# Performance work log

Hardware: AMD Instinct MI355X
Metric: run time of the kernel (lower is better)

Reference implementation:

```python
import jax, jax.numpy as jnp
import numpy as np

N_HEADS = 16
NEG_BIAS = -1e9


def setup_inputs() -> dict:
    key = jax.random.key(0)
    kq, kk, kv = jax.random.split(key, 3)
    B, S, D = 2, 2048, 1024
    queries = jax.random.normal(kq, (B, S, D), dtype=jnp.float32)
    keys = jax.random.normal(kk, (B, S, D), dtype=jnp.float32)
    values = jax.random.normal(kv, (B, S, D), dtype=jnp.float32)
    # causal mask [B, S, S]: True = attend allowed
    mask = jnp.broadcast_to(jnp.tril(jnp.ones((S, S), dtype=bool)), (B, S, S))
    return {"queries": queries, "keys": keys, "values": values, "mask": mask}


def reference(queries, keys, values, mask):
    B, S, D = queries.shape
    H = N_HEADS
    dh = D // H

    def split_heads(t):  # [B,S,D] -> [B,H,S,dh]
        return t.reshape(B, -1, H, dh).transpose(0, 2, 1, 3)

    q = split_heads(queries)
    k = split_heads(keys)
    v = split_heads(values)

    # scaled dot-product similarity: [B,H,Sq,Sk]
    sim = jnp.einsum('bhqd,bhkd->bhqk', q, k) / jnp.sqrt(jnp.asarray(dh, q.dtype))

    # additive mask bias (mask rank 3 -> broadcast over heads)
    bias = NEG_BIAS * (~mask).astype(sim.dtype)  # [B,Sq,Sk]
    masked = sim + bias[:, None, :, :]

    # stable softmax (original subtracts row max then softmaxes)
    weights = jax.nn.softmax(masked, axis=-1)

    # dropout is identity at inference (rate=None -> 0)
    out = jnp.einsum('bhqk,bhkd->bhqd', weights, v)

    # combine heads: [B,H,S,dh] -> [B,S,D]
    out = out.transpose(0, 2, 1, 3).reshape(B, S, D)
    return out
```

## Files before the change

kernel.cpp:

```cpp
#include <hip/hip_runtime.h>

#define B_ 2
#define S_ 2048
#define D_ 1024
#define H_ 16
#define DH 64
#define KB 64
#define SCALE 0.125f

typedef _Float16 f16x8 __attribute__((ext_vector_type(8)));
typedef _Float16 f16x4 __attribute__((ext_vector_type(4)));
typedef float f32x4 __attribute__((ext_vector_type(4)));


__global__ __launch_bounds__(256, 2) void mha_fwd(
    const float* __restrict__ qg, const float* __restrict__ kg,
    const float* __restrict__ vg, float* __restrict__ out)
{
  __shared__ __align__(16) _Float16 lds_k[KB * DH];
  __shared__ __align__(16) _Float16 lds_v[DH * KB];

  int bx = blockIdx.x;
  int L  = (bx & 7) * 64 + (bx >> 3);
  int bh  = L >> 4;
  int qbp = L & 15;
  int h = bh & 15;
  int b = bh >> 4;

  int tid  = threadIdx.x;
  int wid  = tid >> 6;
  int lane = tid & 63;
  int n    = lane & 15;
  int g    = lane >> 4;

  const float* qbase = qg + (size_t)b * S_ * D_ + h * DH;
  const float* kbase = kg + (size_t)b * S_ * D_ + h * DH;
  const float* vbase = vg + (size_t)b * S_ * D_ + h * DH;

  const int skey  = tid >> 2;
  const int spart = tid & 3;
  const int vdh   = tid & 63;
  const int vkq   = tid >> 6;

  float4 kf[4];
  float  vf[16];

  for (int ph = 0; ph < 2; ++ph) {
    const int qb   = ph ? (31 - qbp) : qbp;
    const int nkt  = qb + 1;
    const int qrow = qb * 64 + wid * 16;

    f16x8 bq[2];
    {
      const float* qp = qbase + (size_t)(qrow + n) * D_ + g * 8;
#pragma unroll
      for (int c = 0; c < 2; ++c) {
        float4 x0 = *(const float4*)(qp + c * 32);
        float4 x1 = *(const float4*)(qp + c * 32 + 4);
        f16x8 a;
        a[0]=(_Float16)(x0.x*SCALE); a[1]=(_Float16)(x0.y*SCALE);
        a[2]=(_Float16)(x0.z*SCALE); a[3]=(_Float16)(x0.w*SCALE);
        a[4]=(_Float16)(x1.x*SCALE); a[5]=(_Float16)(x1.y*SCALE);
        a[6]=(_Float16)(x1.z*SCALE); a[7]=(_Float16)(x1.w*SCALE);
        bq[c] = a;
      }
    }

    f32x4 o_acc[4] = {};
    float m_run = -1e30f, l_run = 0.f;

    {
      const float* kp = kbase + (size_t)skey * D_ + spart * 16;
#pragma unroll
      for (int i = 0; i < 4; ++i) kf[i] = ((const float4*)kp)[i];
      const float* vp = vbase + (size_t)(vkq * 16) * D_ + vdh;
#pragma unroll
      for (int j = 0; j < 16; ++j) vf[j] = vp[(size_t)j * D_];
    }

    for (int kt = 0; kt < nkt; ++kt) {
      __syncthreads();
      {
        const float* kfl = (const float*)kf;
        f16x8 h0, h1;
#pragma unroll
        for (int j = 0; j < 8; ++j) { h0[j] = (_Float16)kfl[j]; h1[j] = (_Float16)kfl[8+j]; }
        int c0 = spart * 2;
        *(f16x8*)((char*)lds_k + skey*128 + (((c0  ) ^ (skey&7))<<4)) = h0;
        *(f16x8*)((char*)lds_k + skey*128 + (((c0+1) ^ (skey&7))<<4)) = h1;
      }
      {
        f16x8 h0, h1;
#pragma unroll
        for (int j = 0; j < 8; ++j) { h0[j] = (_Float16)vf[j]; h1[j] = (_Float16)vf[8+j]; }
        int kb8 = vkq * 2;
        _Float16* vt = lds_v + vdh * 64;
        *(f16x8*)(vt + (((kb8  ) ^ (vdh&7)) << 3)) = h0;
        *(f16x8*)(vt + (((kb8+1) ^ (vdh&7)) << 3)) = h1;
      }
      __syncthreads();
      if (kt + 1 < nkt) {
        const float* kp = kbase + (size_t)((kt+1)*KB + skey) * D_ + spart * 16;
#pragma unroll
        for (int i = 0; i < 4; ++i) kf[i] = ((const float4*)kp)[i];
        const float* vp = vbase + (size_t)((kt+1)*KB + vkq*16) * D_ + vdh;
#pragma unroll
        for (int j = 0; j < 16; ++j) vf[j] = vp[(size_t)j * D_];
      }

      f32x4 sc[4] = {};
#pragma unroll
      for (int t = 0; t < 4; ++t) {
        int keyl = t * 16 + n;
#pragma unroll
        for (int c = 0; c < 2; ++c) {
          int off = keyl * 128 + (((c*4+g) ^ (keyl&7)) << 4);
          f16x8 ak = *(f16x8*)((char*)lds_k + off);
          sc[t] = __builtin_amdgcn_mfma_f32_16x16x32_f16(ak, bq[c], sc[t], 0, 0, 0);
        }
      }

      if (kt == nkt - 1) {
        int q = qrow + n;
#pragma unroll
        for (int t = 0; t < 4; ++t)
#pragma unroll
          for (int r = 0; r < 4; ++r) {
            int key = kt*KB + t*16 + 4*g + r;
            if (key > q) sc[t][r] = -1e30f;
          }
      }

      float mx = sc[0][0];
#pragma unroll
      for (int t = 0; t < 4; ++t)
#pragma unroll
        for (int r = 0; r < 4; ++r) mx = fmaxf(mx, sc[t][r]);
      mx = fmaxf(mx, __shfl_xor(mx, 16, 64));
      mx = fmaxf(mx, __shfl_xor(mx, 32, 64));
      float mnew  = fmaxf(m_run, mx);
      float alpha = __expf(m_run - mnew);
      m_run = mnew;
      float s = 0.f;
#pragma unroll
      for (int t = 0; t < 4; ++t)
#pragma unroll
        for (int r = 0; r < 4; ++r) {
          float p = __expf(sc[t][r] - mnew);
          sc[t][r] = p; s += p;
        }
      l_run = l_run * alpha + s;

      float ar[4];
#pragma unroll
      for (int r = 0; r < 4; ++r) ar[r] = __shfl(alpha, 4*g + r, 64);
#pragma unroll
      for (int nt = 0; nt < 4; ++nt) {
        f32x4 oa = o_acc[nt];
#pragma unroll
        for (int r = 0; r < 4; ++r) oa[r] *= ar[r];
        o_acc[nt] = oa;
      }

      f16x4 pa[4];
#pragma unroll
      for (int u = 0; u < 4; ++u) {
        f16x4 p4;
#pragma unroll
        for (int r = 0; r < 4; ++r) p4[r] = (_Float16)sc[u][r];
        pa[u] = p4;
      }

#pragma unroll
      for (int u = 0; u < 4; ++u) {
#pragma unroll
        for (int nt = 0; nt < 4; ++nt) {
          int dh  = nt*16 + n;
          int off = dh*64 + (((2*u + (g>>1)) ^ (n & 7)) << 3) + ((g & 1) << 2);
          f16x4 bv = *(f16x4*)(lds_v + off);
          o_acc[nt] = __builtin_amdgcn_mfma_f32_16x16x16f16(pa[u], bv, o_acc[nt], 0, 0, 0);
        }
      }
    }

    float lsum = l_run;
    lsum += __shfl_xor(lsum, 16, 64);
    lsum += __shfl_xor(lsum, 32, 64);
    float linv[4];
#pragma unroll
    for (int r = 0; r < 4; ++r) linv[r] = 1.0f / __shfl(lsum, 4*g + r, 64);

    float* ob = out + ((size_t)b * S_ + qrow) * D_ + h * DH;
#pragma unroll
    for (int r = 0; r < 4; ++r) {
      float* op = ob + (size_t)(4*g + r) * D_ + n;
#pragma unroll
      for (int nt = 0; nt < 4; ++nt)
        op[nt*16] = o_acc[nt][r] * linv[r];
    }
  }
}

extern "C" void kernel_launch(void* const* d_in, const int* in_sizes, int n_in,
                              void* d_out, int out_size, void* d_ws, size_t ws_size,
                              hipStream_t stream) {
  const float* q = (const float*)d_in[0];
  const float* k = (const float*)d_in[1];
  const float* v = (const float*)d_in[2];
  float* out = (float*)d_out;
  dim3 grid(512);
  mha_fwd<<<grid, 256, 0, stream>>>(q, k, v, out);
}
```

Before: 150.6 us.

## Double-buffer K/V tiles in LDS and add lazy softmax rescaling with exp2

K/V tiles now go into two LDS buffers. The next tile is loaded from global before compute and written to the other buffer afterward, which cuts the loop from two barriers to one. Softmax now uses exp2 with log2e folded into the Q scale. The running max is updated only when some lane's tile max exceeds it by more than a threshold, which skips most rescales of the output accumulator. s_setprio raises wave priority around the MFMA section; the trade-off is doubled LDS use and possible fp16 overflow risk bounded by the threshold.

```diff
diff --git a/kernel.cpp b/kernel.cpp
--- a/kernel.cpp
+++ b/kernel.cpp
@@ -6,7 +6,8 @@
 #define H_ 16
 #define DH 64
 #define KB 64
-#define SCALE 0.125f
+#define SCALE_LOG2 0.18033688011112042f
+#define THR 11.0f
 
 typedef _Float16 f16x8 __attribute__((ext_vector_type(8)));
 typedef _Float16 f16x4 __attribute__((ext_vector_type(4)));
@@ -17,8 +18,8 @@
     const float* __restrict__ qg, const float* __restrict__ kg,
     const float* __restrict__ vg, float* __restrict__ out)
 {
-  __shared__ __align__(16) _Float16 lds_k[KB * DH];
-  __shared__ __align__(16) _Float16 lds_v[DH * KB];
+  __shared__ __align__(16) _Float16 lds_k[2][KB * DH];
+  __shared__ __align__(16) _Float16 lds_v[2][DH * KB];
 
   int bx = blockIdx.x;
   int L  = (bx & 7) * 64 + (bx >> 3);
@@ -45,6 +46,33 @@
   float4 kf[4];
   float  vf[16];
 
+  auto load_tile = [&](int kt) {
+    const float* kp = kbase + (size_t)(kt * KB + skey) * D_ + spart * 16;
+#pragma unroll
+    for (int i = 0; i < 4; ++i) kf[i] = ((const float4*)kp)[i];
+    const float* vp = vbase + (size_t)(kt * KB + vkq * 16) * D_ + vdh;
+#pragma unroll
+    for (int j = 0; j < 16; ++j) vf[j] = vp[(size_t)j * D_];
+  };
+
+  auto store_tile = [&](int buf) {
+    const float* kfl = (const float*)kf;
+    f16x8 h0, h1;
+#pragma unroll
+    for (int j = 0; j < 8; ++j) { h0[j] = (_Float16)kfl[j]; h1[j] = (_Float16)kfl[8 + j]; }
+    int c0 = spart * 2;
+    char* kb_ = (char*)&lds_k[buf][0];
+    *(f16x8*)(kb_ + skey * 128 + (((c0    ) ^ (skey & 7)) << 4)) = h0;
+    *(f16x8*)(kb_ + skey * 128 + (((c0 + 1) ^ (skey & 7)) << 4)) = h1;
+    f16x8 v0, v1;
+#pragma unroll
+    for (int j = 0; j < 8; ++j) { v0[j] = (_Float16)vf[j]; v1[j] = (_Float16)vf[8 + j]; }
+    int kb8 = vkq * 2;
+    _Float16* vt = &lds_v[buf][0] + vdh * 64;
+    *(f16x8*)(vt + (((kb8    ) ^ (vdh & 7)) << 3)) = v0;
+    *(f16x8*)(vt + (((kb8 + 1) ^ (vdh & 7)) << 3)) = v1;
+  };
+
   for (int ph = 0; ph < 2; ++ph) {
     const int qb   = ph ? (31 - qbp) : qbp;
     const int nkt  = qb + 1;
@@ -58,64 +86,35 @@
         float4 x0 = *(const float4*)(qp + c * 32);
         float4 x1 = *(const float4*)(qp + c * 32 + 4);
         f16x8 a;
-        a[0]=(_Float16)(x0.x*SCALE); a[1]=(_Float16)(x0.y*SCALE);
-        a[2]=(_Float16)(x0.z*SCALE); a[3]=(_Float16)(x0.w*SCALE);
-        a[4]=(_Float16)(x1.x*SCALE); a[5]=(_Float16)(x1.y*SCALE);
-        a[6]=(_Float16)(x1.z*SCALE); a[7]=(_Float16)(x1.w*SCALE);
+        a[0]=(_Float16)(x0.x*SCALE_LOG2); a[1]=(_Float16)(x0.y*SCALE_LOG2);
+        a[2]=(_Float16)(x0.z*SCALE_LOG2); a[3]=(_Float16)(x0.w*SCALE_LOG2);
+        a[4]=(_Float16)(x1.x*SCALE_LOG2); a[5]=(_Float16)(x1.y*SCALE_LOG2);
+        a[6]=(_Float16)(x1.z*SCALE_LOG2); a[7]=(_Float16)(x1.w*SCALE_LOG2);
         bq[c] = a;
       }
     }
 
     f32x4 o_acc[4] = {};
-    float m_run = -1e30f, l_run = 0.f;
-
-    {
-      const float* kp = kbase + (size_t)skey * D_ + spart * 16;
-#pragma unroll
-      for (int i = 0; i < 4; ++i) kf[i] = ((const float4*)kp)[i];
-      const float* vp = vbase + (size_t)(vkq * 16) * D_ + vdh;
-#pragma unroll
-      for (int j = 0; j < 16; ++j) vf[j] = vp[(size_t)j * D_];
-    }
+    float m_run = 0.f, l_run = 0.f;
+
+    load_tile(0);
+    store_tile(0);
+    __syncthreads();
+    int cur = 0;
 
     for (int kt = 0; kt < nkt; ++kt) {
-      __syncthreads();
-      {
-        const float* kfl = (const float*)kf;
-        f16x8 h0, h1;
-#pragma unroll
-        for (int j = 0; j < 8; ++j) { h0[j] = (_Float16)kfl[j]; h1[j] = (_Float16)kfl[8+j]; }
-        int c0 = spart * 2;
-        *(f16x8*)((char*)lds_k + skey*128 + (((c0  ) ^ (skey&7))<<4)) = h0;
-        *(f16x8*)((char*)lds_k + skey*128 + (((c0+1) ^ (skey&7))<<4)) = h1;
-      }
-      {
-        f16x8 h0, h1;
-#pragma unroll
-        for (int j = 0; j < 8; ++j) { h0[j] = (_Float16)vf[j]; h1[j] = (_Float16)vf[8+j]; }
-        int kb8 = vkq * 2;
-        _Float16* vt = lds_v + vdh * 64;
-        *(f16x8*)(vt + (((kb8  ) ^ (vdh&7)) << 3)) = h0;
-        *(f16x8*)(vt + (((kb8+1) ^ (vdh&7)) << 3)) = h1;
-      }
-      __syncthreads();
-      if (kt + 1 < nkt) {
-        const float* kp = kbase + (size_t)((kt+1)*KB + skey) * D_ + spart * 16;
-#pragma unroll
-        for (int i = 0; i < 4; ++i) kf[i] = ((const float4*)kp)[i];
-        const float* vp = vbase + (size_t)((kt+1)*KB + vkq*16) * D_ + vdh;
-#pragma unroll
-        for (int j = 0; j < 16; ++j) vf[j] = vp[(size_t)j * D_];
-      }
-
+      if (kt + 1 < nkt) load_tile(kt + 1);
+
+      __builtin_amdgcn_s_setprio(1);
+      const char* kb_ = (const char*)&lds_k[cur][0];
       f32x4 sc[4] = {};
 #pragma unroll
       for (int t = 0; t < 4; ++t) {
         int keyl = t * 16 + n;
 #pragma unroll
         for (int c = 0; c < 2; ++c) {
-          int off = keyl * 128 + (((c*4+g) ^ (keyl&7)) << 4);
-          f16x8 ak = *(f16x8*)((char*)lds_k + off);
+          int off = keyl * 128 + (((c * 4 + g) ^ (keyl & 7)) << 4);
+          f16x8 ak = *(f16x8*)(kb_ + off);
           sc[t] = __builtin_amdgcn_mfma_f32_16x16x32_f16(ak, bq[c], sc[t], 0, 0, 0);
         }
       }
@@ -126,41 +125,48 @@
         for (int t = 0; t < 4; ++t)
 #pragma unroll
           for (int r = 0; r < 4; ++r) {
-            int key = kt*KB + t*16 + 4*g + r;
+            int key = kt * KB + t * 16 + 4 * g + r;
             if (key > q) sc[t][r] = -1e30f;
           }
       }
 
-      float mx = sc[0][0];
+      float mxt[4];
 #pragma unroll
       for (int t = 0; t < 4; ++t)
-#pragma unroll
-        for (int r = 0; r < 4; ++r) mx = fmaxf(mx, sc[t][r]);
+        mxt[t] = fmaxf(fmaxf(sc[t][0], sc[t][1]), fmaxf(sc[t][2], sc[t][3]));
+      float mx = fmaxf(fmaxf(mxt[0], mxt[1]), fmaxf(mxt[2], mxt[3]));
       mx = fmaxf(mx, __shfl_xor(mx, 16, 64));
       mx = fmaxf(mx, __shfl_xor(mx, 32, 64));
-      float mnew  = fmaxf(m_run, mx);
-      float alpha = __expf(m_run - mnew);
-      m_run = mnew;
+
       float s = 0.f;
 #pragma unroll
-      for (int t = 0; t < 4; ++t)
-#pragma unroll
-        for (int r = 0; r < 4; ++r) {
-          float p = __expf(sc[t][r] - mnew);
-          sc[t][r] = p; s += p;
-        }
-      l_run = l_run * alpha + s;
-
-      float ar[4];
-#pragma unroll
-      for (int r = 0; r < 4; ++r) ar[r] = __shfl(alpha, 4*g + r, 64);
-#pragma unroll
-      for (int nt = 0; nt < 4; ++nt) {
-        f32x4 oa = o_acc[nt];
-#pragma unroll
-        for (int r = 0; r < 4; ++r) oa[r] *= ar[r];
-        o_acc[nt] = oa;
-      }
+      for (int t = 0; t < 4; ++t) {
+        f32x4 p = sc[t];
+#pragma unroll
+        for (int r = 0; r < 4; ++r) p[r] = exp2f(p[r] - m_run);
+        sc[t] = p;
+        s += (p[0] + p[1]) + (p[2] + p[3]);
+      }
+
+      if (!__all(mx <= m_run + THR)) {
+        float mnew  = fmaxf(m_run, mx);
+        float alpha = exp2f(m_run - mnew);
+#pragma unroll
+        for (int t = 0; t < 4; ++t)
+#pragma unroll
+          for (int r = 0; r < 4; ++r) sc[t][r] *= alpha;
+        s *= alpha;
+        l_run *= alpha;
+        m_run = mnew;
+        float ar[4];
+#pragma unroll
+        for (int r = 0; r < 4; ++r) ar[r] = __shfl(alpha, 4 * g + r, 64);
+#pragma unroll
+        for (int nt = 0; nt < 4; ++nt)
+#pragma unroll
+          for (int r = 0; r < 4; ++r) o_acc[nt][r] *= ar[r];
+      }
+      l_run += s;
 
       f16x4 pa[4];
 #pragma unroll
@@ -171,16 +177,22 @@
         pa[u] = p4;
       }
 
+      const _Float16* vb_ = &lds_v[cur][0];
 #pragma unroll
       for (int u = 0; u < 4; ++u) {
 #pragma unroll
         for (int nt = 0; nt < 4; ++nt) {
-          int dh  = nt*16 + n;
-          int off = dh*64 + (((2*u + (g>>1)) ^ (n & 7)) << 3) + ((g & 1) << 2);
-          f16x4 bv = *(f16x4*)(lds_v + off);
+          int dhv = nt * 16 + n;
+          int off = dhv * 64 + ((((2 * u + (g >> 1)) ^ (n & 7))) << 3) + ((g & 1) << 2);
+          f16x4 bv = *(f16x4*)(vb_ + off);
           o_acc[nt] = __builtin_amdgcn_mfma_f32_16x16x16f16(pa[u], bv, o_acc[nt], 0, 0, 0);
         }
       }
+      __builtin_amdgcn_s_setprio(0);
+
+      if (kt + 1 < nkt) store_tile(cur ^ 1);
+      __syncthreads();
+      cur ^= 1;
     }
 
     float lsum = l_run;
@@ -188,15 +200,15 @@
     lsum += __shfl_xor(lsum, 32, 64);
     float linv[4];
 #pragma unroll
-    for (int r = 0; r < 4; ++r) linv[r] = 1.0f / __shfl(lsum, 4*g + r, 64);
+    for (int r = 0; r < 4; ++r) linv[r] = 1.0f / __shfl(lsum, 4 * g + r, 64);
 
     float* ob = out + ((size_t)b * S_ + qrow) * D_ + h * DH;
 #pragma unroll
     for (int r = 0; r < 4; ++r) {
-      float* op = ob + (size_t)(4*g + r) * D_ + n;
+      float* op = ob + (size_t)(4 * g + r) * D_ + n;
 #pragma unroll
       for (int nt = 0; nt < 4; ++nt)
-        op[nt*16] = o_acc[nt][r] * linv[r];
+        op[nt * 16] = o_acc[nt][r] * linv[r];
     }
   }
 }
```

After: 156.1 us. 3.7% more time.
